# Optimization experiments

Measured on AMD Instinct MI355X. Metric: run time of the kernel, lower is better.

## Reference

```python
import jax, jax.numpy as jnp
import numpy as np

H = 4        # num_heads
DH = 64      # output_dim (d_head)
D = 256      # input_dim (hidden)
NUM_LAYERS = 2


def _gru_cell(x, h, Wih, Whh, bih, bhh):
    # PyTorch GRUCell: gates ordered (r, z, n)
    gi = x @ Wih.T + bih
    gh = h @ Whh.T + bhh
    i_r, i_z, i_n = jnp.split(gi, 3, axis=-1)
    h_r, h_z, h_n = jnp.split(gh, 3, axis=-1)
    r = jax.nn.sigmoid(i_r + h_r)
    z = jax.nn.sigmoid(i_z + h_z)
    n = jnp.tanh(i_n + r * h_n)
    return (1.0 - z) * n + z * h


def _mha(x, attn_mask, Wq, bq, Wk, bk, Wv, bv, Wo):
    B, N, _ = x.shape
    q = (x @ Wq.T + bq).reshape(B, N, H, DH)
    k = (x @ Wk.T + bk).reshape(B, N, H, DH)
    v = (x @ Wv.T + bv).reshape(B, N, H, DH)
    # scores computed in fp32 (autocast disabled in original)
    scores = jnp.einsum('bnhd,bmhd->bhnm', q.astype(jnp.float32), k.astype(jnp.float32)) / jnp.float32(DH) ** 0.5
    scores = jnp.where(attn_mask[:, None], jnp.float32(-1e9), scores)  # mask broadcast over heads
    attn = jax.nn.softmax(scores, axis=-1)
    ctx = jnp.einsum('bhnm,bmhd->bnhd', attn, v).reshape(B, N, H * DH)
    return ctx @ Wo.T  # W_O has no bias


def setup_inputs() -> dict:
    B, N = 1024, 128
    key = jax.random.key(0)
    ks = jax.random.split(key, 14)
    s = 0.02
    return {
        'latent': jax.random.normal(ks[0], (B, N, D), jnp.float32),
        'comm_mask': jax.random.randint(ks[1], (B, N, N), 0, 2) > 0,
        'trait_weight': jax.random.normal(ks[2], (B, N), jnp.float32),
        'Wq': jax.random.normal(ks[3], (H * DH, D), jnp.float32) * s,
        'bq': jnp.zeros((H * DH,), jnp.float32),
        'Wk': jax.random.normal(ks[4], (H * DH, D), jnp.float32) * s,
        'bk': jnp.zeros((H * DH,), jnp.float32),
        'Wv': jax.random.normal(ks[5], (H * DH, D), jnp.float32) * s,
        'bv': jnp.zeros((H * DH,), jnp.float32),
        'Wo': jax.random.normal(ks[6], (DH, H * DH), jnp.float32) * s,
        'Wih': jax.random.normal(ks[7], (3 * D, DH), jnp.float32) * s,
        'Whh': jax.random.normal(ks[8], (3 * D, D), jnp.float32) * s,
        'bih': jnp.zeros((3 * D,), jnp.float32),
        'bhh': jnp.zeros((3 * D,), jnp.float32),
    }


def reference(latent, comm_mask, trait_weight, Wq, bq, Wk, bk, Wv, bv, Wo, Wih, Whh, bih, bhh):
    B, N, _ = latent.shape
    attn_mask = ~comm_mask                                    # [B,N,N] True = blocked
    update_mask = (comm_mask.sum(axis=-1) > 1)[..., None]     # [B,N,1]
    for _ in range(NUM_LAYERS):
        info = _mha(latent, attn_mask, Wq, bq, Wk, bk, Wv, bv, Wo)          # [B,N,DH]
        upd = _gru_cell(info.reshape(-1, DH), latent.reshape(-1, D), Wih, Whh, bih, bhh)
        latent = jnp.where(update_mask, upd.reshape(B, N, D), latent)
    return latent
```

## Files before the change

### kernel.cpp

```cpp
#include <hip/hip_runtime.h>
#include <stdint.h>

#define NTOK 128
#define DHID 256
#define NHEAD 4
#define DHEAD 64

typedef short bf16x8 __attribute__((ext_vector_type(8)));
typedef float f32x4 __attribute__((ext_vector_type(4)));

#define MFMA(a,b,c) __builtin_amdgcn_mfma_f32_16x16x32_bf16((a),(b),(c),0,0,0)

__device__ __forceinline__ float bf2f(uint16_t u){
  union { uint32_t i; float f; } v; v.i = ((uint32_t)u) << 16; return v.f;
}
__device__ __forceinline__ uint16_t f2bf(float f){
  union { uint32_t i; float f; } v; v.f = f;
  uint32_t i = v.i + 0x7FFFu + ((v.i >> 16) & 1u);
  return (uint16_t)(i >> 16);
}

__global__ void k_detect(const uint32_t* __restrict__ raw, uint32_t* __restrict__ flag){
  int lane = threadIdx.x;
  int hits = 0;
  #pragma unroll
  for (int i = 0; i < 16; i++){
    uint32_t w = raw[lane*16 + i];
    uint32_t e = (w >> 7) & 0xFFu;
    hits += (e >= 0x70u && e <= 0x8Fu) ? 1 : 0;
  }
  #pragma unroll
  for (int m = 1; m < 64; m <<= 1) hits += __shfl_xor(hits, m);
  if (lane == 0) *flag = (hits > 512) ? 1u : 0u;
}

__global__ void k_conv(const void* __restrict__ src, unsigned long long off,
                       uint16_t* __restrict__ dst, const uint32_t* __restrict__ flag, int n){
  const int isbf = (int)*flag;
  int i0 = (blockIdx.x * blockDim.x + threadIdx.x) * 8;
  int stride = gridDim.x * blockDim.x * 8;
  if (isbf){
    const uint16_t* s = (const uint16_t*)src + off;
    for (int i = i0; i < n; i += stride)
      *(bf16x8*)(dst + i) = *(const bf16x8*)(s + i);
  } else {
    const float* s = (const float*)src + off;
    for (int i = i0; i < n; i += stride){
      float4 a = *(const float4*)(s + i);
      float4 b = *(const float4*)(s + i + 4);
      uint16_t o[8] = {f2bf(a.x),f2bf(a.y),f2bf(a.z),f2bf(a.w),
                       f2bf(b.x),f2bf(b.y),f2bf(b.z),f2bf(b.w)};
      *(bf16x8*)(dst + i) = *(const bf16x8*)o;
    }
  }
}

__global__ void k_store(const uint16_t* __restrict__ L, void* __restrict__ dst,
                        unsigned long long off, const uint32_t* __restrict__ flag, int n){
  const int isbf = (int)*flag;
  int i0 = (blockIdx.x * blockDim.x + threadIdx.x) * 8;
  int stride = gridDim.x * blockDim.x * 8;
  if (isbf){
    uint16_t* d = (uint16_t*)dst + off;
    for (int i = i0; i < n; i += stride)
      *(bf16x8*)(d + i) = *(const bf16x8*)(L + i);
  } else {
    float* d = (float*)dst + off;
    for (int i = i0; i < n; i += stride){
      bf16x8 v = *(const bf16x8*)(L + i);
      #pragma unroll
      for (int e = 0; e < 8; e++) d[i + e] = bf2f((uint16_t)v[e]);
    }
  }
}

__global__ __launch_bounds__(256) void k_maskpack(const int* __restrict__ mask,
                                                  unsigned long long* __restrict__ packed,
                                                  unsigned char* __restrict__ upd, int nrows){
  int row = blockIdx.x * 4 + (threadIdx.x >> 6);
  if (row >= nrows) return;
  int lane = threadIdx.x & 63;
  const int* mrow = mask + (size_t)row * NTOK;
  unsigned long long b0 = __ballot(mrow[lane] != 0);
  unsigned long long b1 = __ballot(mrow[lane + 64] != 0);
  if (lane == 0){
    packed[row*2 + 0] = b0;
    packed[row*2 + 1] = b1;
    upd[row] = (unsigned char)((__popcll(b0) + __popcll(b1)) > 1 ? 1 : 0);
  }
}

__global__ __launch_bounds__(256) void k_qkv(
    const uint16_t* __restrict__ X,
    const uint16_t* __restrict__ Wq, const uint16_t* __restrict__ bq,
    const uint16_t* __restrict__ Wk, const uint16_t* __restrict__ bk,
    const uint16_t* __restrict__ Wv, const uint16_t* __restrict__ bv,
    uint16_t* __restrict__ Oq, uint16_t* __restrict__ Ok, uint16_t* __restrict__ Ov)
{
  extern __shared__ uint16_t sm[];
  uint16_t* Xs = sm;
  uint16_t* Ws = sm + 64*256;
  const int r0 = blockIdx.x * 64;
  const int tid = threadIdx.x;
  const int lane = tid & 63, lr = lane & 15, lg = lane >> 4;
  const int wav = tid >> 6;
  const int wr = (wav >> 1) * 32, wc = (wav & 1) * 32;

  #pragma unroll
  for (int i = 0; i < 8; i++){
    int c = tid + i*256, row = c >> 5, g = c & 31;
    *(bf16x8*)(Xs + row*256 + (g ^ (row & 7))*8) =
        *(const bf16x8*)(X + (size_t)(r0+row)*DHID + g*8);
  }

  bf16x8 wreg[8];
  auto wptr = [&](int t)->const uint16_t*{
    int w = t >> 2;
    return (w == 0) ? Wq : ((w == 1) ? Wk : Wv);
  };
  auto preload = [&](int t){
    const uint16_t* W = wptr(t);
    int c0t = (t & 3) * 64;
    #pragma unroll
    for (int i = 0; i < 8; i++){
      int idx = tid + i*256, r = idx >> 5, g = idx & 31;
      wreg[i] = *(const bf16x8*)(W + (size_t)(c0t + r)*DHID + g*8);
    }
  };
  preload(0);

  for (int t = 0; t < 12; t++){
    __syncthreads();
    #pragma unroll
    for (int i = 0; i < 8; i++){
      int idx = tid + i*256, r = idx >> 5, g = idx & 31;
      *(bf16x8*)(Ws + r*256 + ((g ^ (r & 7))*8)) = wreg[i];
    }
    __syncthreads();
    if (t < 11) preload(t+1);

    f32x4 acc[2][2] = {};
    #pragma unroll
    for (int kk = 0; kk < 8; kk++){
      int off = ((kk*4 + lg) ^ (lr & 7)) * 8;
      bf16x8 a0 = *(const bf16x8*)(Xs + (wr +      lr)*256 + off);
      bf16x8 a1 = *(const bf16x8*)(Xs + (wr + 16 + lr)*256 + off);
      bf16x8 b0 = *(const bf16x8*)(Ws + (wc +      lr)*256 + off);
      bf16x8 b1 = *(const bf16x8*)(Ws + (wc + 16 + lr)*256 + off);
      acc[0][0] = MFMA(a0, b0, acc[0][0]);
      acc[0][1] = MFMA(a0, b1, acc[0][1]);
      acc[1][0] = MFMA(a1, b0, acc[1][0]);
      acc[1][1] = MFMA(a1, b1, acc[1][1]);
    }
    int w = t >> 2, c0t = (t & 3) * 64;
    const uint16_t* bias = (w == 0) ? bq : ((w == 1) ? bk : bv);
    uint16_t* O = (w == 0) ? Oq : ((w == 1) ? Ok : Ov);
    #pragma unroll
    for (int i = 0; i < 2; i++)
    #pragma unroll
    for (int j = 0; j < 2; j++){
      int col = c0t + wc + j*16 + lr;
      float bvv = bf2f(bias[col]);
      #pragma unroll
      for (int rr = 0; rr < 4; rr++){
        int row = r0 + wr + i*16 + lg*4 + rr;
        O[(size_t)row*DHID + col] = f2bf(acc[i][j][rr] + bvv);
      }
    }
  }
}

__global__ __launch_bounds__(256) void k_attn(
    const uint16_t* __restrict__ Q, const uint16_t* __restrict__ Kb, const uint16_t* __restrict__ V,
    const unsigned long long* __restrict__ packed, uint16_t* __restrict__ ctx)
{
  extern __shared__ uint16_t sm[];
  uint16_t* Ks = sm;
  uint16_t* Vt = sm + 128*64;
  uint16_t* Ps = Vt + 64*128;
  const int b = blockIdx.x >> 2;
  const int h = blockIdx.x & 3;
  const int tid = threadIdx.x, lane = tid & 63, wav = tid >> 6;
  const int lr = lane & 15, lg = lane >> 4;
  const size_t base = ((size_t)b * NTOK) * DHID + h * DHEAD;

  #pragma unroll
  for (int i = 0; i < 4; i++){
    int c = tid + i*256;
    int row = c >> 3, g = c & 7;
    *(bf16x8*)(Ks + row*64 + (g ^ (row & 7))*8) =
        *(const bf16x8*)(Kb + base + (size_t)row*DHID + g*8);
  }
  #pragma unroll
  for (int i = 0; i < 4; i++){
    int c = tid + i*256;
    int n = c & 127, d8 = (c >> 7) * 8;
    bf16x8 v = *(const bf16x8*)(V + base + (size_t)n*DHID + d8);
    #pragma unroll
    for (int e = 0; e < 8; e++){
      int d = d8 + e;
      Vt[d*128 + ((n >> 3) ^ (d & 7))*8 + (n & 7)] = (uint16_t)v[e];
    }
  }
  __syncthreads();

  const int qrow0 = wav * 32;
  bf16x8 qf[2][2];
  #pragma unroll
  for (int i = 0; i < 2; i++)
  #pragma unroll
  for (int kk = 0; kk < 2; kk++)
    qf[i][kk] = *(const bf16x8*)(Q + base + (size_t)(qrow0 + i*16 + lr)*DHID + kk*32 + lg*8);

  f32x4 sa[2][8] = {};
  #pragma unroll
  for (int kk = 0; kk < 2; kk++){
    int off = ((kk*4 + lg) ^ (lr & 7)) * 8;
    #pragma unroll
    for (int j = 0; j < 8; j++){
      bf16x8 bf = *(const bf16x8*)(Ks + (j*16 + lr)*64 + off);
      sa[0][j] = MFMA(qf[0][kk], bf, sa[0][j]);
      sa[1][j] = MFMA(qf[1][kk], bf, sa[1][j]);
    }
  }
  #pragma unroll
  for (int i = 0; i < 2; i++){
    #pragma unroll
    for (int rr = 0; rr < 4; rr++){
      int n = qrow0 + i*16 + lg*4 + rr;
      unsigned long long m0 = packed[((size_t)b*NTOK + n)*2 + 0];
      unsigned long long m1 = packed[((size_t)b*NTOK + n)*2 + 1];
      float sv[8];
      float mx = -3.0e38f;
      #pragma unroll
      for (int j = 0; j < 8; j++){
        int col = j*16 + lr;
        unsigned long long w = (col < 64) ? m0 : m1;
        float s = sa[i][j][rr] * 0.125f;
        sv[j] = ((w >> (col & 63)) & 1ull) ? s : -1e9f;
        mx = fmaxf(mx, sv[j]);
      }
      mx = fmaxf(mx, __shfl_xor(mx, 1));
      mx = fmaxf(mx, __shfl_xor(mx, 2));
      mx = fmaxf(mx, __shfl_xor(mx, 4));
      mx = fmaxf(mx, __shfl_xor(mx, 8));
      float sum = 0.f;
      #pragma unroll
      for (int j = 0; j < 8; j++){ sv[j] = __expf(sv[j] - mx); sum += sv[j]; }
      sum += __shfl_xor(sum, 1);
      sum += __shfl_xor(sum, 2);
      sum += __shfl_xor(sum, 4);
      sum += __shfl_xor(sum, 8);
      float inv = __builtin_amdgcn_rcpf(sum);
      #pragma unroll
      for (int j = 0; j < 8; j++){
        int col = j*16 + lr;
        Ps[n*128 + ((col >> 3) ^ (n & 7))*8 + (col & 7)] = f2bf(sv[j] * inv);
      }
    }
  }
  __syncthreads();

  f32x4 oa[2][4] = {};
  #pragma unroll
  for (int kk = 0; kk < 4; kk++){
    int off = ((kk*4 + lg) ^ (lr & 7)) * 8;
    bf16x8 a0 = *(const bf16x8*)(Ps + (qrow0 +      lr)*128 + off);
    bf16x8 a1 = *(const bf16x8*)(Ps + (qrow0 + 16 + lr)*128 + off);
    #pragma unroll
    for (int j = 0; j < 4; j++){
      bf16x8 bf = *(const bf16x8*)(Vt + (j*16 + lr)*128 + off);
      oa[0][j] = MFMA(a0, bf, oa[0][j]);
      oa[1][j] = MFMA(a1, bf, oa[1][j]);
    }
  }
  #pragma unroll
  for (int i = 0; i < 2; i++)
  #pragma unroll
  for (int j = 0; j < 4; j++)
  #pragma unroll
  for (int rr = 0; rr < 4; rr++){
    int n = qrow0 + i*16 + lg*4 + rr;
    ctx[((size_t)b*NTOK + n)*DHID + h*DHEAD + j*16 + lr] = f2bf(oa[i][j][rr]);
  }
}

__global__ __launch_bounds__(256, 2) void k_gru(
    const uint16_t* __restrict__ ctxp, const uint16_t* __restrict__ lat,
    const uint16_t* __restrict__ Wo, const uint16_t* __restrict__ Wih, const uint16_t* __restrict__ Whh,
    const uint16_t* __restrict__ bih, const uint16_t* __restrict__ bhh,
    const unsigned char* __restrict__ upd, uint16_t* __restrict__ lat_out)
{
  extern __shared__ uint16_t sm[];
  uint16_t* Wb0   = sm;
  uint16_t* Wb1   = sm + 15360;
  uint16_t* Is    = sm + 30720;
  uint16_t* biasS = sm + 38912;
  const int r0 = blockIdx.x * 128;
  const int tid = threadIdx.x, lane = tid & 63, wav = tid >> 6;
  const int lr = lane & 15, lg = lane >> 4;
  const int wrow = wav * 32;

  #pragma unroll
  for (int i = 0; i < 6; i++){
    int idx = tid + i*256;
    if (idx < 1536) biasS[idx] = (idx < 768) ? bih[idx] : bhh[idx - 768];
  }

  auto stage_async = [&](int cs, uint16_t* buf){
    #pragma unroll
    for (int c = 0; c < 7; c++){
      int G = c*256 + tid;
      const uint16_t* src;
      if (G < 1536){
        int r = G >> 5, gp = G & 31;
        src = Whh + (size_t)((r>>4)*256 + cs*16 + (r&15))*DHID + (gp ^ (r&7))*8;
      } else {
        int G2 = G - 1536, r = G2 >> 3, gp = G2 & 7;
        src = Wih + (size_t)((r>>4)*256 + cs*16 + (r&15))*DHEAD + (gp ^ (r&7))*8;
      }
      __builtin_amdgcn_global_load_lds(
          (const __attribute__((address_space(1))) uint32_t*)src,
          (__attribute__((address_space(3))) uint32_t*)(buf + (size_t)G*8),
          16, 0, 0);
    }
    if (tid < 128){
      int G = 1792 + tid;
      int G2 = G - 1536, r = G2 >> 3, gp = G2 & 7;
      const uint16_t* src = Wih + (size_t)((r>>4)*256 + cs*16 + (r&15))*DHEAD + (gp ^ (r&7))*8;
      __builtin_amdgcn_global_load_lds(
          (const __attribute__((address_space(1))) uint32_t*)src,
          (__attribute__((address_space(3))) uint32_t*)(buf + (size_t)G*8),
          16, 0, 0);
    }
  };

  stage_async(0, Wb0);

  f32x4 ai[2][4] = {};
  #pragma unroll
  for (int kk = 0; kk < 8; kk++){
    bf16x8 bw[4];
    #pragma unroll
    for (int j = 0; j < 4; j++)
      bw[j] = *(const bf16x8*)(Wo + (size_t)(j*16 + lr)*DHID + kk*32 + lg*8);
    #pragma unroll
    for (int t = 0; t < 2; t++){
      bf16x8 ac = *(const bf16x8*)(ctxp + (size_t)(r0 + wrow + t*16 + lr)*DHID + kk*32 + lg*8);
      #pragma unroll
      for (int j = 0; j < 4; j++) ai[t][j] = MFMA(ac, bw[j], ai[t][j]);
    }
  }
  #pragma unroll
  for (int t = 0; t < 2; t++)
  #pragma unroll
  for (int j = 0; j < 4; j++)
  #pragma unroll
  for (int rr = 0; rr < 4; rr++){
    int row = wrow + t*16 + lg*4 + rr, col = j*16 + lr;
    Is[row*64 + ((col>>3) ^ (row&7))*8 + (col&7)] = f2bf(ai[t][j][rr]);
  }

  bf16x8 aL[2][8];
  #pragma unroll
  for (int t = 0; t < 2; t++)
  #pragma unroll
  for (int kk = 0; kk < 8; kk++)
    aL[t][kk] = *(const bf16x8*)(lat + (size_t)(r0 + wrow + t*16 + lr)*DHID + kk*32 + lg*8);

  uint32_t u4[2];
  #pragma unroll
  for (int t = 0; t < 2; t++)
    u4[t] = *(const uint32_t*)(upd + r0 + wrow + t*16 + lg*4);

  __syncthreads();

  const float LOG2E = 1.44269504f;
  for (int cs = 0; cs < 16; cs++){
    uint16_t* Wcur = (cs & 1) ? Wb1 : Wb0;
    if (cs < 15) stage_async(cs+1, (cs & 1) ? Wb0 : Wb1);

    const uint16_t* WhhS = Wcur;
    const uint16_t* WihS = Wcur + 12288;

    f32x4 arz[2][2] = {};
    f32x4 gin[2] = {}, ghn[2] = {};

    #pragma unroll
    for (int kk = 0; kk < 2; kk++){
      int off = ((kk*4 + lg) ^ (lr & 7)) * 8;
      bf16x8 br = *(const bf16x8*)(WihS + (0*16 + lr)*64 + off);
      bf16x8 bz = *(const bf16x8*)(WihS + (1*16 + lr)*64 + off);
      bf16x8 bn = *(const bf16x8*)(WihS + (2*16 + lr)*64 + off);
      #pragma unroll
      for (int t = 0; t < 2; t++){
        bf16x8 a = *(const bf16x8*)(Is + (wrow + t*16 + lr)*64 + off);
        arz[0][t] = MFMA(a, br, arz[0][t]);
        arz[1][t] = MFMA(a, bz, arz[1][t]);
        gin[t]    = MFMA(a, bn, gin[t]);
      }
    }
    #pragma unroll
    for (int kk = 0; kk < 8; kk++){
      int off = ((kk*4 + lg) ^ (lr & 7)) * 8;
      bf16x8 br = *(const bf16x8*)(WhhS + (0*16 + lr)*256 + off);
      bf16x8 bz = *(const bf16x8*)(WhhS + (1*16 + lr)*256 + off);
      bf16x8 bn = *(const bf16x8*)(WhhS + (2*16 + lr)*256 + off);
      #pragma unroll
      for (int t = 0; t < 2; t++){
        arz[0][t] = MFMA(aL[t][kk], br, arz[0][t]);
        arz[1][t] = MFMA(aL[t][kk], bz, arz[1][t]);
        ghn[t]    = MFMA(aL[t][kk], bn, ghn[t]);
      }
    }

    int col = cs*16 + lr;
    float brz0 = bf2f(biasS[col])     + bf2f(biasS[768+col]);
    float brz1 = bf2f(biasS[256+col]) + bf2f(biasS[1024+col]);
    float bin_ = bf2f(biasS[512+col]);
    float bhn  = bf2f(biasS[1280+col]);
    #pragma unroll
    for (int t = 0; t < 2; t++)
    #pragma unroll
    for (int rr = 0; rr < 4; rr++){
      int row = wrow + t*16 + lg*4 + rr;
      float hv = bf2f(lat[(size_t)(r0+row)*DHID + col]);
      float xr = arz[0][t][rr] + brz0;
      float xz = arz[1][t][rr] + brz1;
      float rg = __builtin_amdgcn_rcpf(1.f + __builtin_amdgcn_exp2f(-xr*LOG2E));
      float zg = __builtin_amdgcn_rcpf(1.f + __builtin_amdgcn_exp2f(-xz*LOG2E));
      float nx = (gin[t][rr] + bin_) + rg*(ghn[t][rr] + bhn);
      nx = fminf(10.f, fmaxf(-10.f, nx));
      float e2 = __builtin_amdgcn_exp2f(-2.f*LOG2E*nx);
      float ng = (1.f - e2) * __builtin_amdgcn_rcpf(1.f + e2);
      float hp = (1.f - zg)*ng + zg*hv;
      float ov = ((u4[t] >> (rr*8)) & 1u) ? hp : hv;
      lat_out[(size_t)(r0+row)*DHID + col] = f2bf(ov);
    }
    __syncthreads();
  }
}

extern "C" void kernel_launch(void* const* d_in, const int* in_sizes, int n_in,
                              void* d_out, int out_size, void* d_ws, size_t ws_size,
                              hipStream_t stream)
{
  (void)in_sizes; (void)n_in; (void)out_size;
  const void* latent = d_in[0];
  const int*  mask   = (const int*)d_in[1];
  const void* Wq  = d_in[3]; const void* bq  = d_in[4];
  const void* Wk  = d_in[5]; const void* bk  = d_in[6];
  const void* Wv  = d_in[7]; const void* bv  = d_in[8];
  const void* Wo  = d_in[9];
  const void* Wih = d_in[10]; const void* Whh = d_in[11];
  const void* bih = d_in[12]; const void* bhh = d_in[13];

  uint8_t* p = (uint8_t*)d_ws;
  uint32_t* flag = (uint32_t*)p;            p += 256;
  uint16_t* Wqc  = (uint16_t*)p;            p += 65536*2;
  uint16_t* Wkc  = (uint16_t*)p;            p += 65536*2;
  uint16_t* Wvc  = (uint16_t*)p;            p += 65536*2;
  uint16_t* Woc  = (uint16_t*)p;            p += 16384*2;
  uint16_t* Wihc = (uint16_t*)p;            p += 49152*2;
  uint16_t* Whhc = (uint16_t*)p;            p += 196608*2;
  uint16_t* bqc  = (uint16_t*)p;            p += 512;
  uint16_t* bkc  = (uint16_t*)p;            p += 512;
  uint16_t* bvc  = (uint16_t*)p;            p += 512;
  uint16_t* bihc = (uint16_t*)p;            p += 1536;
  uint16_t* bhhc = (uint16_t*)p;            p += 1536;
  uint8_t* chunk0 = p;
  size_t reserved = (size_t)(chunk0 - (uint8_t*)d_ws);
  const size_t perb = 5ull*65536 + 2048 + 128;

  const int Btot = 1024;
  int CB = (int)((ws_size > reserved ? ws_size - reserved : 0) / perb);
  if (CB > Btot) CB = Btot;
  if (CB < 1)    CB = 1;

  auto cgrid = [](int n){ int b = (n/8 + 255)/256; if (b > 2048) b = 2048; if (b < 1) b = 1; return (unsigned)b; };

  k_detect<<<1, 64, 0, stream>>>((const uint32_t*)latent, flag);
  k_conv<<<cgrid(65536), 256, 0, stream>>>(Wq, 0, Wqc, flag, 65536);
  k_conv<<<cgrid(65536), 256, 0, stream>>>(Wk, 0, Wkc, flag, 65536);
  k_conv<<<cgrid(65536), 256, 0, stream>>>(Wv, 0, Wvc, flag, 65536);
  k_conv<<<cgrid(16384), 256, 0, stream>>>(Wo, 0, Woc, flag, 16384);
  k_conv<<<cgrid(49152), 256, 0, stream>>>(Wih, 0, Wihc, flag, 49152);
  k_conv<<<cgrid(196608),256, 0, stream>>>(Whh, 0, Whhc, flag, 196608);
  k_conv<<<1, 256, 0, stream>>>(bq, 0, bqc, flag, 256);
  k_conv<<<1, 256, 0, stream>>>(bk, 0, bkc, flag, 256);
  k_conv<<<1, 256, 0, stream>>>(bv, 0, bvc, flag, 256);
  k_conv<<<1, 256, 0, stream>>>(bih, 0, bihc, flag, 768);
  k_conv<<<1, 256, 0, stream>>>(bhh, 0, bhhc, flag, 768);

  for (int b0 = 0; b0 < Btot; b0 += CB){
    int cb = (Btot - b0 < CB) ? (Btot - b0) : CB;
    int rows = cb * 128;
    int nelem = rows * DHID;
    uint8_t* q = chunk0;
    uint16_t* L    = (uint16_t*)q; q += (size_t)cb*65536;
    uint16_t* q_ws = (uint16_t*)q; q += (size_t)cb*65536;
    uint16_t* k_ws = (uint16_t*)q; q += (size_t)cb*65536;
    uint16_t* v_ws = (uint16_t*)q; q += (size_t)cb*65536;
    uint16_t* c_ws = (uint16_t*)q; q += (size_t)cb*65536;
    unsigned long long* packed = (unsigned long long*)q; q += (size_t)cb*2048;
    unsigned char* updp = (unsigned char*)q;

    k_conv<<<cgrid(nelem), 256, 0, stream>>>(latent, (unsigned long long)b0*NTOK*DHID, L, flag, nelem);
    k_maskpack<<<dim3(rows/4), 256, 0, stream>>>(mask + (size_t)b0*NTOK*NTOK, packed, updp, rows);

    for (int layer = 0; layer < 2; layer++){
      k_qkv <<<dim3(rows/64),  256, 65536, stream>>>(L, Wqc,bqc, Wkc,bkc, Wvc,bvc, q_ws, k_ws, v_ws);
      k_attn<<<dim3(cb*NHEAD), 256, 65536, stream>>>(q_ws, k_ws, v_ws, packed, c_ws);
      k_gru <<<dim3(rows/128), 256, 80896, stream>>>(c_ws, L, Woc, Wihc, Whhc, bihc, bhhc, updp, L);
    }
    k_store<<<cgrid(nelem), 256, 0, stream>>>(L, d_out, (unsigned long long)b0*NTOK*DHID, flag, nelem);
  }
}
```

Measured before the change: 721.5 us.

## Enlarge QKV tiles, stage mask in LDS, defer softmax normalization, skip bf16 copies

The QKV projection kernel moves to 512-thread blocks computing 128x128 output tiles, so it runs 6 weight stages instead of 12 and reuses each weight tile across more rows. The attention kernel now loads the packed mask into shared memory once and applies the softmax reciprocal to the output context instead of to each probability. A device-side pointer table lets kernels read bf16 inputs directly and skip the conversion and store copies when inputs are already bf16. The larger tiles raise shared memory per block to 128 KB and increase register pressure, which limits occupancy.

Measured after the change: 806.5 us. 11.8% more time.

```diff
diff --git a/kernel.cpp b/kernel.cpp
--- a/kernel.cpp
+++ b/kernel.cpp
@@ -34,43 +34,55 @@
   if (lane == 0) *flag = (hits > 512) ? 1u : 0u;
 }
 
+__global__ void k_setptrs(const uint32_t* __restrict__ flag, void** __restrict__ tab,
+  const void* latent, const void* Wq, const void* bq, const void* Wk, const void* bk,
+  const void* Wv, const void* bv, const void* Wo, const void* Wih, const void* Whh,
+  const void* bih, const void* bhh, void* dout,
+  const uint16_t* L, const uint16_t* Wqc, const uint16_t* bqc, const uint16_t* Wkc,
+  const uint16_t* bkc, const uint16_t* Wvc, const uint16_t* bvc, const uint16_t* Woc,
+  const uint16_t* Wihc, const uint16_t* Whhc, const uint16_t* bihc, const uint16_t* bhhc)
+{
+  int f = (int)*flag;
+  tab[0]  = f ? (void*)latent : (void*)L;
+  tab[1]  = f ? (void*)Wq  : (void*)Wqc;
+  tab[2]  = f ? (void*)bq  : (void*)bqc;
+  tab[3]  = f ? (void*)Wk  : (void*)Wkc;
+  tab[4]  = f ? (void*)bk  : (void*)bkc;
+  tab[5]  = f ? (void*)Wv  : (void*)Wvc;
+  tab[6]  = f ? (void*)bv  : (void*)bvc;
+  tab[7]  = f ? (void*)Wo  : (void*)Woc;
+  tab[8]  = f ? (void*)Wih : (void*)Wihc;
+  tab[9]  = f ? (void*)Whh : (void*)Whhc;
+  tab[10] = f ? (void*)bih : (void*)bihc;
+  tab[11] = f ? (void*)bhh : (void*)bhhc;
+  tab[12] = f ? dout : (void*)L;
+}
+
 __global__ void k_conv(const void* __restrict__ src, unsigned long long off,
                        uint16_t* __restrict__ dst, const uint32_t* __restrict__ flag, int n){
-  const int isbf = (int)*flag;
+  if (*flag) return;
   int i0 = (blockIdx.x * blockDim.x + threadIdx.x) * 8;
   int stride = gridDim.x * blockDim.x * 8;
-  if (isbf){
-    const uint16_t* s = (const uint16_t*)src + off;
-    for (int i = i0; i < n; i += stride)
-      *(bf16x8*)(dst + i) = *(const bf16x8*)(s + i);
-  } else {
-    const float* s = (const float*)src + off;
-    for (int i = i0; i < n; i += stride){
-      float4 a = *(const float4*)(s + i);
-      float4 b = *(const float4*)(s + i + 4);
-      uint16_t o[8] = {f2bf(a.x),f2bf(a.y),f2bf(a.z),f2bf(a.w),
-                       f2bf(b.x),f2bf(b.y),f2bf(b.z),f2bf(b.w)};
-      *(bf16x8*)(dst + i) = *(const bf16x8*)o;
-    }
+  const float* s = (const float*)src + off;
+  for (int i = i0; i < n; i += stride){
+    float4 a = *(const float4*)(s + i);
+    float4 b = *(const float4*)(s + i + 4);
+    uint16_t o[8] = {f2bf(a.x),f2bf(a.y),f2bf(a.z),f2bf(a.w),
+                     f2bf(b.x),f2bf(b.y),f2bf(b.z),f2bf(b.w)};
+    *(bf16x8*)(dst + i) = *(const bf16x8*)o;
   }
 }
 
 __global__ void k_store(const uint16_t* __restrict__ L, void* __restrict__ dst,
                         unsigned long long off, const uint32_t* __restrict__ flag, int n){
-  const int isbf = (int)*flag;
+  if (*flag) return;
   int i0 = (blockIdx.x * blockDim.x + threadIdx.x) * 8;
   int stride = gridDim.x * blockDim.x * 8;
-  if (isbf){
-    uint16_t* d = (uint16_t*)dst + off;
-    for (int i = i0; i < n; i += stride)
-      *(bf16x8*)(d + i) = *(const bf16x8*)(L + i);
-  } else {
-    float* d = (float*)dst + off;
-    for (int i = i0; i < n; i += stride){
-      bf16x8 v = *(const bf16x8*)(L + i);
-      #pragma unroll
-      for (int e = 0; e < 8; e++) d[i + e] = bf2f((uint16_t)v[e]);
-    }
+  float* d = (float*)dst + off;
+  for (int i = i0; i < n; i += stride){
+    bf16x8 v = *(const bf16x8*)(L + i);
+    #pragma unroll
+    for (int e = 0; e < 8; e++) d[i + e] = bf2f((uint16_t)v[e]);
   }
 }
 
@@ -90,75 +102,75 @@
   }
 }
 
-__global__ __launch_bounds__(256) void k_qkv(
-    const uint16_t* __restrict__ X,
-    const uint16_t* __restrict__ Wq, const uint16_t* __restrict__ bq,
-    const uint16_t* __restrict__ Wk, const uint16_t* __restrict__ bk,
-    const uint16_t* __restrict__ Wv, const uint16_t* __restrict__ bv,
+__global__ __launch_bounds__(512, 2) void k_qkv(
+    void* const* __restrict__ tab, const uint16_t* __restrict__ L, int layer,
     uint16_t* __restrict__ Oq, uint16_t* __restrict__ Ok, uint16_t* __restrict__ Ov)
 {
   extern __shared__ uint16_t sm[];
   uint16_t* Xs = sm;
-  uint16_t* Ws = sm + 64*256;
-  const int r0 = blockIdx.x * 64;
+  uint16_t* Ws = sm + 128*256;
+  const uint16_t* X  = (layer == 0) ? (const uint16_t*)tab[0] : L;
+  const uint16_t* Wq = (const uint16_t*)tab[1];
+  const uint16_t* bq = (const uint16_t*)tab[2];
+  const uint16_t* Wk = (const uint16_t*)tab[3];
+  const uint16_t* bk = (const uint16_t*)tab[4];
+  const uint16_t* Wv = (const uint16_t*)tab[5];
+  const uint16_t* bv = (const uint16_t*)tab[6];
+  const int r0 = blockIdx.x * 128;
   const int tid = threadIdx.x;
   const int lane = tid & 63, lr = lane & 15, lg = lane >> 4;
   const int wav = tid >> 6;
-  const int wr = (wav >> 1) * 32, wc = (wav & 1) * 32;
+  const int wr = (wav >> 1) * 32, wc = (wav & 1) * 64;
 
   #pragma unroll
   for (int i = 0; i < 8; i++){
-    int c = tid + i*256, row = c >> 5, g = c & 31;
+    int c = tid + i*512, row = c >> 5, g = c & 31;
     *(bf16x8*)(Xs + row*256 + (g ^ (row & 7))*8) =
         *(const bf16x8*)(X + (size_t)(r0+row)*DHID + g*8);
   }
 
   bf16x8 wreg[8];
-  auto wptr = [&](int t)->const uint16_t*{
-    int w = t >> 2;
-    return (w == 0) ? Wq : ((w == 1) ? Wk : Wv);
-  };
   auto preload = [&](int t){
-    const uint16_t* W = wptr(t);
-    int c0t = (t & 3) * 64;
+    const uint16_t* W = (t < 2) ? Wq : ((t < 4) ? Wk : Wv);
+    int c0t = (t & 1) * 128;
     #pragma unroll
     for (int i = 0; i < 8; i++){
-      int idx = tid + i*256, r = idx >> 5, g = idx & 31;
+      int idx = tid + i*512, r = idx >> 5, g = idx & 31;
       wreg[i] = *(const bf16x8*)(W + (size_t)(c0t + r)*DHID + g*8);
     }
   };
   preload(0);
 
-  for (int t = 0; t < 12; t++){
+  for (int t = 0; t < 6; t++){
     __syncthreads();
     #pragma unroll
     for (int i = 0; i < 8; i++){
-      int idx = tid + i*256, r = idx >> 5, g = idx & 31;
+      int idx = tid + i*512, r = idx >> 5, g = idx & 31;
       *(bf16x8*)(Ws + r*256 + ((g ^ (r & 7))*8)) = wreg[i];
     }
     __syncthreads();
-    if (t < 11) preload(t+1);
-
-    f32x4 acc[2][2] = {};
+    if (t < 5) preload(t+1);
+
+    f32x4 acc[2][4] = {};
     #pragma unroll
     for (int kk = 0; kk < 8; kk++){
       int off = ((kk*4 + lg) ^ (lr & 7)) * 8;
       bf16x8 a0 = *(const bf16x8*)(Xs + (wr +      lr)*256 + off);
       bf16x8 a1 = *(const bf16x8*)(Xs + (wr + 16 + lr)*256 + off);
-      bf16x8 b0 = *(const bf16x8*)(Ws + (wc +      lr)*256 + off);
-      bf16x8 b1 = *(const bf16x8*)(Ws + (wc + 16 + lr)*256 + off);
-      acc[0][0] = MFMA(a0, b0, acc[0][0]);
-      acc[0][1] = MFMA(a0, b1, acc[0][1]);
-      acc[1][0] = MFMA(a1, b0, acc[1][0]);
-      acc[1][1] = MFMA(a1, b1, acc[1][1]);
-    }
-    int w = t >> 2, c0t = (t & 3) * 64;
-    const uint16_t* bias = (w == 0) ? bq : ((w == 1) ? bk : bv);
-    uint16_t* O = (w == 0) ? Oq : ((w == 1) ? Ok : Ov);
+      #pragma unroll
+      for (int j = 0; j < 4; j++){
+        bf16x8 b = *(const bf16x8*)(Ws + (wc + j*16 + lr)*256 + off);
+        acc[0][j] = MFMA(a0, b, acc[0][j]);
+        acc[1][j] = MFMA(a1, b, acc[1][j]);
+      }
+    }
+    const uint16_t* bias = (t < 2) ? bq : ((t < 4) ? bk : bv);
+    uint16_t* O = (t < 2) ? Oq : ((t < 4) ? Ok : Ov);
+    int c0t = (t & 1) * 128;
     #pragma unroll
     for (int i = 0; i < 2; i++)
     #pragma unroll
-    for (int j = 0; j < 2; j++){
+    for (int j = 0; j < 4; j++){
       int col = c0t + wc + j*16 + lr;
       float bvv = bf2f(bias[col]);
       #pragma unroll
@@ -178,12 +190,14 @@
   uint16_t* Ks = sm;
   uint16_t* Vt = sm + 128*64;
   uint16_t* Ps = Vt + 64*128;
+  unsigned long long* Ms = (unsigned long long*)(Ps + 128*128);
   const int b = blockIdx.x >> 2;
   const int h = blockIdx.x & 3;
   const int tid = threadIdx.x, lane = tid & 63, wav = tid >> 6;
   const int lr = lane & 15, lg = lane >> 4;
   const size_t base = ((size_t)b * NTOK) * DHID + h * DHEAD;
 
+  Ms[tid] = packed[(size_t)b*NTOK*2 + tid];
   #pragma unroll
   for (int i = 0; i < 4; i++){
     int c = tid + i*256;
@@ -223,13 +237,14 @@
       sa[1][j] = MFMA(qf[1][kk], bf, sa[1][j]);
     }
   }
+  float iv[2][4];
   #pragma unroll
   for (int i = 0; i < 2; i++){
     #pragma unroll
     for (int rr = 0; rr < 4; rr++){
       int n = qrow0 + i*16 + lg*4 + rr;
-      unsigned long long m0 = packed[((size_t)b*NTOK + n)*2 + 0];
-      unsigned long long m1 = packed[((size_t)b*NTOK + n)*2 + 1];
+      unsigned long long m0 = Ms[n*2 + 0];
+      unsigned long long m1 = Ms[n*2 + 1];
       float sv[8];
       float mx = -3.0e38f;
       #pragma unroll
@@ -251,11 +266,11 @@
       sum += __shfl_xor(sum, 2);
       sum += __shfl_xor(sum, 4);
       sum += __shfl_xor(sum, 8);
-      float inv = __builtin_amdgcn_rcpf(sum);
+      iv[i][rr] = __builtin_amdgcn_rcpf(sum);
       #pragma unroll
       for (int j = 0; j < 8; j++){
         int col = j*16 + lr;
-        Ps[n*128 + ((col >> 3) ^ (n & 7))*8 + (col & 7)] = f2bf(sv[j] * inv);
+        Ps[n*128 + ((col >> 3) ^ (n & 7))*8 + (col & 7)] = f2bf(sv[j]);
       }
     }
   }
@@ -281,21 +296,26 @@
   #pragma unroll
   for (int rr = 0; rr < 4; rr++){
     int n = qrow0 + i*16 + lg*4 + rr;
-    ctx[((size_t)b*NTOK + n)*DHID + h*DHEAD + j*16 + lr] = f2bf(oa[i][j][rr]);
+    ctx[((size_t)b*NTOK + n)*DHID + h*DHEAD + j*16 + lr] = f2bf(oa[i][j][rr] * iv[i][rr]);
   }
 }
 
 __global__ __launch_bounds__(256, 2) void k_gru(
-    const uint16_t* __restrict__ ctxp, const uint16_t* __restrict__ lat,
-    const uint16_t* __restrict__ Wo, const uint16_t* __restrict__ Wih, const uint16_t* __restrict__ Whh,
-    const uint16_t* __restrict__ bih, const uint16_t* __restrict__ bhh,
-    const unsigned char* __restrict__ upd, uint16_t* __restrict__ lat_out)
+    void* const* __restrict__ tab, const uint16_t* __restrict__ L, int layer,
+    const uint16_t* __restrict__ ctxp, const unsigned char* __restrict__ upd)
 {
   extern __shared__ uint16_t sm[];
   uint16_t* Wb0   = sm;
   uint16_t* Wb1   = sm + 15360;
   uint16_t* Is    = sm + 30720;
   uint16_t* biasS = sm + 38912;
+  const uint16_t* lat = (layer == 0) ? (const uint16_t*)tab[0] : L;
+  uint16_t* lat_out   = (layer == 0) ? (uint16_t*)L : (uint16_t*)tab[12];
+  const uint16_t* Wo  = (const uint16_t*)tab[7];
+  const uint16_t* Wih = (const uint16_t*)tab[8];
+  const uint16_t* Whh = (const uint16_t*)tab[9];
+  const uint16_t* bih = (const uint16_t*)tab[10];
+  const uint16_t* bhh = (const uint16_t*)tab[11];
   const int r0 = blockIdx.x * 128;
   const int tid = threadIdx.x, lane = tid & 63, wav = tid >> 6;
   const int lr = lane & 15, lg = lane >> 4;
@@ -457,6 +477,7 @@
 
   uint8_t* p = (uint8_t*)d_ws;
   uint32_t* flag = (uint32_t*)p;            p += 256;
+  void** ptab    = (void**)p;               p += 256;
   uint16_t* Wqc  = (uint16_t*)p;            p += 65536*2;
   uint16_t* Wkc  = (uint16_t*)p;            p += 65536*2;
   uint16_t* Wvc  = (uint16_t*)p;            p += 65536*2;
@@ -505,14 +526,21 @@
     unsigned long long* packed = (unsigned long long*)q; q += (size_t)cb*2048;
     unsigned char* updp = (unsigned char*)q;
 
-    k_conv<<<cgrid(nelem), 256, 0, stream>>>(latent, (unsigned long long)b0*NTOK*DHID, L, flag, nelem);
+    const float* lat_f32 = (const float*)latent + (size_t)b0*NTOK*DHID;
+    const uint16_t* lat_bf = (const uint16_t*)latent + (size_t)b0*NTOK*DHID;
+    void* dout_b = (void*)((uint16_t*)d_out + (size_t)b0*NTOK*DHID);
+
+    k_setptrs<<<1, 1, 0, stream>>>(flag, ptab,
+        (const void*)lat_bf, Wq, bq, Wk, bk, Wv, bv, Wo, Wih, Whh, bih, bhh, dout_b,
+        L, Wqc, bqc, Wkc, bkc, Wvc, bvc, Woc, Wihc, Whhc, bihc, bhhc);
+    k_conv<<<cgrid(nelem), 256, 0, stream>>>((const void*)lat_f32, 0, L, flag, nelem);
     k_maskpack<<<dim3(rows/4), 256, 0, stream>>>(mask + (size_t)b0*NTOK*NTOK, packed, updp, rows);
 
     for (int layer = 0; layer < 2; layer++){
-      k_qkv <<<dim3(rows/64),  256, 65536, stream>>>(L, Wqc,bqc, Wkc,bkc, Wvc,bvc, q_ws, k_ws, v_ws);
-      k_attn<<<dim3(cb*NHEAD), 256, 65536, stream>>>(q_ws, k_ws, v_ws, packed, c_ws);
-      k_gru <<<dim3(rows/128), 256, 80896, stream>>>(c_ws, L, Woc, Wihc, Whhc, bihc, bhhc, updp, L);
-    }
-    k_store<<<cgrid(nelem), 256, 0, stream>>>(L, d_out, (unsigned long long)b0*NTOK*DHID, flag, nelem);
-  }
-}
+      k_qkv <<<dim3(rows/128), 512, 131072, stream>>>(ptab, L, layer, q_ws, k_ws, v_ws);
+      k_attn<<<dim3(cb*NHEAD), 256, 67584,  stream>>>(q_ws, k_ws, v_ws, packed, c_ws);
+      k_gru <<<dim3(rows/128), 256, 80896,  stream>>>(ptab, L, layer, c_ws, updp);
+    }
+    k_store<<<cgrid(nelem), 256, 0, stream>>>(L, (void*)((float*)d_out + (size_t)b0*NTOK*DHID), 0, flag, nelem);
+  }
+}
```
